# Optimization experiments

Hardware: AMD Instinct MI355X
Metric: run time of the kernel (lower is better)

The kernel has to match this reference:

```python
import jax, jax.numpy as jnp
import numpy as np

N_NODES = 100000
N_EDGES = 1600000
D = 128
K = 3
LEAKY_ALPHA = 0.2  # tf.nn.leaky_relu default
L2_EPS = 1e-12     # tf.math.l2_normalize default


def spmm(row, col, val, x, n_nodes):
    # y[r] = sum_{e: row[e]==r} val[e] * x[col[e]]
    return jax.ops.segment_sum(val[:, None] * x[col], row, num_segments=n_nodes)


def setup_inputs() -> dict:
    key = jax.random.key(0)
    ks = jax.random.split(key, 8)
    embeddings = jax.random.normal(ks[0], (N_NODES, D), dtype=jnp.float32) * 0.1
    edge_row = jax.random.randint(ks[1], (N_EDGES,), 0, N_NODES, dtype=jnp.int32)
    edge_col = jax.random.randint(ks[2], (N_EDGES,), 0, N_NODES, dtype=jnp.int32)
    # normalized-laplacian-like positive weights
    edge_val = jax.random.uniform(ks[3], (N_EDGES,), dtype=jnp.float32) * 0.05
    W_gc = jax.random.normal(ks[4], (K, D, D), dtype=jnp.float32) * (1.0 / np.sqrt(D))
    b_gc = jax.random.normal(ks[5], (K, D), dtype=jnp.float32) * 0.01
    W_bi = jax.random.normal(ks[6], (K, D, D), dtype=jnp.float32) * (1.0 / np.sqrt(D))
    b_bi = jax.random.normal(ks[7], (K, D), dtype=jnp.float32) * 0.01
    return {"embeddings": embeddings, "edge_row": edge_row, "edge_col": edge_col,
            "edge_val": edge_val, "W_gc": W_gc, "b_gc": b_gc, "W_bi": W_bi, "b_bi": b_bi}


def reference(embeddings, edge_row, edge_col, edge_val, W_gc, b_gc, W_bi, b_bi):
    n = embeddings.shape[0]
    x = embeddings
    depth_embeddings = [x]
    for i in range(W_gc.shape[0]):
        Lx = spmm(edge_row, edge_col, edge_val, x, n)   # L @ x  (L has zero diag)
        prop = Lx + x                                    # S @ x, S = L with diag 1
        emb = prop @ W_gc[i] + b_gc[i][None, :]
        bi = (x * Lx) @ W_bi[i] + b_bi[i][None, :]
        x = jax.nn.leaky_relu(emb + bi, negative_slope=LEAKY_ALPHA)
        sq = jnp.sum(x * x, axis=1, keepdims=True)
        norm_x = x / jnp.sqrt(jnp.maximum(sq, L2_EPS))   # tf l2_normalize semantics
        depth_embeddings.append(norm_x)
        x = norm_x  # note: original feeds normalized x to next layer via loop var? see notes
    return jnp.concatenate(depth_embeddings, axis=1)  # [N, (K+1)*D]
```

## Files before the change

### kernel.cpp

```cpp
#include <hip/hip_runtime.h>
#include <hip/hip_bf16.h>

#define ND 128
#define LDO 512
#define ALPHA 0.2f
#define L2EPS 1e-12f
#define SCAN_B 256
#define NCHUNK 256
#define RPB 512

typedef __attribute__((ext_vector_type(8))) short short8;
typedef __attribute__((ext_vector_type(4))) float f32x4;
typedef __attribute__((ext_vector_type(2))) float f32x2;

__device__ __forceinline__ short f2bf(float f) {
    union { float f; unsigned u; } c; c.f = f;
    unsigned u = c.u;
    unsigned r = (u + 0x7fffu + ((u >> 16) & 1u)) >> 16;
    return (short)r;
}
__device__ __forceinline__ float bf2f(unsigned short u) {
    union { unsigned u; float f; } c; c.u = ((unsigned)u) << 16;
    return c.f;
}
__device__ __forceinline__ void gload_lds16(const void* g, void* l) {
    __builtin_amdgcn_global_load_lds(
        (const __attribute__((address_space(1))) unsigned int*)g,
        (__attribute__((address_space(3))) unsigned int*)l, 16, 0, 0);
}

__global__ void copy_emb_kernel(const float* __restrict__ emb, float* __restrict__ out,
                                unsigned short* __restrict__ xb,
                                unsigned int* __restrict__ xf8w, int n) {
    int idx = blockIdx.x * blockDim.x + threadIdx.x;
    int total = n * 32;
    if (idx >= total) return;
    int r = idx >> 5, c4 = idx & 31;
    const float4 v = *reinterpret_cast<const float4*>(emb + (size_t)r * ND + c4 * 4);
    *reinterpret_cast<float4*>(out + (size_t)r * LDO + c4 * 4) = v;
    ushort4 b;
    b.x = (unsigned short)f2bf(v.x); b.y = (unsigned short)f2bf(v.y);
    b.z = (unsigned short)f2bf(v.z); b.w = (unsigned short)f2bf(v.w);
    *reinterpret_cast<ushort4*>(xb + (size_t)r * ND + c4 * 4) = b;
    unsigned int u = __builtin_amdgcn_cvt_pk_fp8_f32(v.x, v.y, 0, false);
    u = __builtin_amdgcn_cvt_pk_fp8_f32(v.z, v.w, u, true);
    xf8w[(size_t)r * 32 + c4] = u;
}

__global__ __launch_bounds__(256) void bucket_hist_kernel(const int* __restrict__ erow,
                                                          int* __restrict__ gcnt,
                                                          int n_edges, int nb, int ch) {
    __shared__ int cnt[256];
    int b = blockIdx.x;
    cnt[threadIdx.x] = 0;
    __syncthreads();
    int s = b * ch, e = min(n_edges, s + ch);
    for (int j = s + threadIdx.x; j < e; j += 256) {
        atomicAdd(&cnt[erow[j] >> 9], 1);
    }
    __syncthreads();
    for (int i = threadIdx.x; i < nb; i += 256) gcnt[i * NCHUNK + b] = cnt[i];
}

__global__ __launch_bounds__(SCAN_B) void scanA_kernel(const int* __restrict__ in,
                                                       int* __restrict__ outp,
                                                       int* __restrict__ partials, int n) {
    __shared__ int sm[SCAN_B];
    int i = blockIdx.x * SCAN_B + threadIdx.x;
    int v = (i < n) ? in[i] : 0;
    sm[threadIdx.x] = v;
    __syncthreads();
#pragma unroll
    for (int off = 1; off < SCAN_B; off <<= 1) {
        int t = (threadIdx.x >= off) ? sm[threadIdx.x - off] : 0;
        __syncthreads();
        sm[threadIdx.x] += t;
        __syncthreads();
    }
    if (i < n) outp[i] = sm[threadIdx.x] - v;
    if (threadIdx.x == SCAN_B - 1) partials[blockIdx.x] = sm[SCAN_B - 1];
}

__global__ __launch_bounds__(512) void scanB_kernel(int* __restrict__ partials, int nb) {
    __shared__ int sm[512];
    int v = (threadIdx.x < nb) ? partials[threadIdx.x] : 0;
    sm[threadIdx.x] = v;
    __syncthreads();
#pragma unroll
    for (int off = 1; off < 512; off <<= 1) {
        int t = (threadIdx.x >= off) ? sm[threadIdx.x - off] : 0;
        __syncthreads();
        sm[threadIdx.x] += t;
        __syncthreads();
    }
    if (threadIdx.x < nb) partials[threadIdx.x] = sm[threadIdx.x] - v;
}

__global__ __launch_bounds__(256) void bucket_scatter_kernel(const int* __restrict__ erow,
                                                             const int* __restrict__ ecol,
                                                             const float* __restrict__ eval,
                                                             const int* __restrict__ gscan,
                                                             const int* __restrict__ part,
                                                             int2* __restrict__ tmp,
                                                             int n_edges, int nb, int ch) {
    __shared__ int cur[256];
    int b = blockIdx.x;
    for (int i = threadIdx.x; i < nb; i += 256)
        cur[i] = gscan[i * NCHUNK + b] + part[i];
    __syncthreads();
    int s = b * ch, e = min(n_edges, s + ch);
    for (int j = s + threadIdx.x; j < e; j += 256) {
        int r = erow[j];
        int pos = atomicAdd(&cur[r >> 9], 1);
        int2 p;
        p.x = ecol[j] | ((r & (RPB - 1)) << 17);
        p.y = __float_as_int(eval[j]);
        tmp[pos] = p;
    }
}

__global__ __launch_bounds__(256) void bucket_sort_kernel(const int2* __restrict__ tmp,
                                                          const int* __restrict__ gscan,
                                                          const int* __restrict__ part,
                                                          int2* __restrict__ pv,
                                                          int* __restrict__ row_start,
                                                          int n, int n_edges, int nb) {
    __shared__ int hist[RPB];
    __shared__ int cur[RPB];
    __shared__ int sc[256];
    const int t = threadIdx.x;
    const int bkt = blockIdx.x;
    const int r0 = bkt << 9;
    const int s = gscan[bkt * NCHUNK] + part[bkt];
    const int e = (bkt + 1 < nb) ? (gscan[(bkt + 1) * NCHUNK] + part[bkt + 1]) : n_edges;

    for (int i = t; i < RPB; i += 256) hist[i] = 0;
    __syncthreads();
    for (int j = s + t; j < e; j += 256) atomicAdd(&hist[tmp[j].x >> 17], 1);
    __syncthreads();
    int a0 = hist[2 * t], a1 = hist[2 * t + 1];
    sc[t] = a0 + a1;
    __syncthreads();
#pragma unroll
    for (int off = 1; off < 256; off <<= 1) {
        int v = (t >= off) ? sc[t - off] : 0;
        __syncthreads();
        sc[t] += v;
        __syncthreads();
    }
    int base = s + sc[t] - a0 - a1;
    cur[2 * t] = base;
    cur[2 * t + 1] = base + a0;
    __syncthreads();
    int r1 = min(n, r0 + RPB);
    for (int i = t; i < r1 - r0; i += 256) row_start[r0 + i] = cur[i];
    if (t == 0 && r1 == n) row_start[n] = n_edges;
    __syncthreads();
    for (int j = s + t; j < e; j += 256) {
        int2 p = tmp[j];
        int pos = atomicAdd(&cur[p.x >> 17], 1);
        int2 q;
        q.x = p.x & 0x1FFFF;
        q.y = p.y;
        pv[pos] = q;
    }
}

__global__ __launch_bounds__(256) void spmm_axm_kernel(const int* __restrict__ row_start,
                                                       const int2* __restrict__ pv,
                                                       const unsigned char* __restrict__ xf8,
                                                       const unsigned short* __restrict__ xb,
                                                       unsigned short* __restrict__ Axm, int n) {
    int r = blockIdx.x * 16 + (threadIdx.x >> 4);
    if (r >= n) return;
    int l = threadIdx.x & 15;
    int s = row_start[r], e = row_start[r + 1];
    float a[8] = {0.f, 0.f, 0.f, 0.f, 0.f, 0.f, 0.f, 0.f};
    int j = s;
    for (; j + 3 < e; j += 4) {
        int2 p0 = pv[j], p1 = pv[j + 1], p2 = pv[j + 2], p3 = pv[j + 3];
        uint2 q0 = *reinterpret_cast<const uint2*>(xf8 + (size_t)p0.x * ND + l * 8);
        uint2 q1 = *reinterpret_cast<const uint2*>(xf8 + (size_t)p1.x * ND + l * 8);
        uint2 q2 = *reinterpret_cast<const uint2*>(xf8 + (size_t)p2.x * ND + l * 8);
        uint2 q3 = *reinterpret_cast<const uint2*>(xf8 + (size_t)p3.x * ND + l * 8);
        float v0 = __int_as_float(p0.y), v1 = __int_as_float(p1.y);
        float v2 = __int_as_float(p2.y), v3 = __int_as_float(p3.y);
        f32x2 g0 = __builtin_amdgcn_cvt_pk_f32_fp8(q0.x, false);
        f32x2 g1 = __builtin_amdgcn_cvt_pk_f32_fp8(q0.x, true);
        f32x2 g2 = __builtin_amdgcn_cvt_pk_f32_fp8(q0.y, false);
        f32x2 g3 = __builtin_amdgcn_cvt_pk_f32_fp8(q0.y, true);
        a[0] += v0 * g0.x; a[1] += v0 * g0.y; a[2] += v0 * g1.x; a[3] += v0 * g1.y;
        a[4] += v0 * g2.x; a[5] += v0 * g2.y; a[6] += v0 * g3.x; a[7] += v0 * g3.y;
        g0 = __builtin_amdgcn_cvt_pk_f32_fp8(q1.x, false);
        g1 = __builtin_amdgcn_cvt_pk_f32_fp8(q1.x, true);
        g2 = __builtin_amdgcn_cvt_pk_f32_fp8(q1.y, false);
        g3 = __builtin_amdgcn_cvt_pk_f32_fp8(q1.y, true);
        a[0] += v1 * g0.x; a[1] += v1 * g0.y; a[2] += v1 * g1.x; a[3] += v1 * g1.y;
        a[4] += v1 * g2.x; a[5] += v1 * g2.y; a[6] += v1 * g3.x; a[7] += v1 * g3.y;
        g0 = __builtin_amdgcn_cvt_pk_f32_fp8(q2.x, false);
        g1 = __builtin_amdgcn_cvt_pk_f32_fp8(q2.x, true);
        g2 = __builtin_amdgcn_cvt_pk_f32_fp8(q2.y, false);
        g3 = __builtin_amdgcn_cvt_pk_f32_fp8(q2.y, true);
        a[0] += v2 * g0.x; a[1] += v2 * g0.y; a[2] += v2 * g1.x; a[3] += v2 * g1.y;
        a[4] += v2 * g2.x; a[5] += v2 * g2.y; a[6] += v2 * g3.x; a[7] += v2 * g3.y;
        g0 = __builtin_amdgcn_cvt_pk_f32_fp8(q3.x, false);
        g1 = __builtin_amdgcn_cvt_pk_f32_fp8(q3.x, true);
        g2 = __builtin_amdgcn_cvt_pk_f32_fp8(q3.y, false);
        g3 = __builtin_amdgcn_cvt_pk_f32_fp8(q3.y, true);
        a[0] += v3 * g0.x; a[1] += v3 * g0.y; a[2] += v3 * g1.x; a[3] += v3 * g1.y;
        a[4] += v3 * g2.x; a[5] += v3 * g2.y; a[6] += v3 * g3.x; a[7] += v3 * g3.y;
    }
    for (; j < e; ++j) {
        int2 p0 = pv[j];
        float v0 = __int_as_float(p0.y);
        uint2 q0 = *reinterpret_cast<const uint2*>(xf8 + (size_t)p0.x * ND + l * 8);
        f32x2 g0 = __builtin_amdgcn_cvt_pk_f32_fp8(q0.x, false);
        f32x2 g1 = __builtin_amdgcn_cvt_pk_f32_fp8(q0.x, true);
        f32x2 g2 = __builtin_amdgcn_cvt_pk_f32_fp8(q0.y, false);
        f32x2 g3 = __builtin_amdgcn_cvt_pk_f32_fp8(q0.y, true);
        a[0] += v0 * g0.x; a[1] += v0 * g0.y;
        a[2] += v0 * g1.x; a[3] += v0 * g1.y;
        a[4] += v0 * g2.x; a[5] += v0 * g2.y;
        a[6] += v0 * g3.x; a[7] += v0 * g3.y;
    }
    short8 xv = *reinterpret_cast<const short8*>(xb + (size_t)r * ND + l * 8);
    short8 prv, xmv;
#pragma unroll
    for (int q = 0; q < 8; ++q) {
        float xf = bf2f((unsigned short)xv[q]);
        prv[q] = f2bf(xf + a[q]);
        xmv[q] = f2bf(xf * a[q]);
    }
    int sz = r & 7;
    unsigned short* rowp = Axm + (size_t)r * 256;
    *reinterpret_cast<short8*>(rowp + ((l        ^ sz) << 3)) = prv;
    *reinterpret_cast<short8*>(rowp + (((16 + l) ^ sz) << 3)) = xmv;
}

__global__ void prep_w_kernel(const float* __restrict__ Wgc, const float* __restrict__ bgc,
                              const float* __restrict__ Wbi, const float* __restrict__ bbi,
                              short* __restrict__ Wt2, float* __restrict__ bsum) {
    int z = blockIdx.x;
    int k = blockIdx.y;
    int t = threadIdx.x;
    int nn = t & 127;
    int h  = (t < 128) ? 0 : 1;
    const float* src = h ? (Wbi + ((size_t)z * 128 + k) * 128)
                         : (Wgc + ((size_t)z * 128 + k) * 128);
    float v = src[nn];
    int idx16 = k >> 3, e8 = k & 7;
    size_t addr = ((size_t)(z * 2 + h) * 128 + nn) * 128 + ((idx16 ^ (nn & 7)) << 3) + e8;
    Wt2[addr] = f2bf(v);
    if (k == 0 && t < 128) bsum[z * 128 + t] = bgc[z * 128 + t] + bbi[z * 128 + t];
}

__global__ __launch_bounds__(256) void fused_layer_mfma(
        const unsigned short* __restrict__ Axm,
        const short* __restrict__ Wt2,
        const float* __restrict__ bsum,
        float* __restrict__ xout,
        unsigned short* __restrict__ xbout,
        unsigned char* __restrict__ xf8out,
        int n) {
    __shared__ short A_lds[64 * 256];
    __shared__ short W_lds[128 * 128];

    const int tid  = threadIdx.x;
    const int row0 = blockIdx.x * 64;
    const int lane = tid & 63;
    const int w    = tid >> 6;
    const int lrow = lane & 15;
    const int kgrp = lane >> 4;

    {
        const char* gA = (const char*)(Axm + (size_t)row0 * 256) + w * 8192 + lane * 16;
        char*       lA = (char*)A_lds + w * 8192;
        const char* gW = (const char*)Wt2 + w * 8192 + lane * 16;
        char*       lW = (char*)W_lds + w * 8192;
#pragma unroll
        for (int it = 0; it < 8; ++it) {
            gload_lds16(gA + it * 1024, lA + it * 1024);
            gload_lds16(gW + it * 1024, lW + it * 1024);
        }
    }
    asm volatile("s_waitcnt vmcnt(0)" ::: "memory");
    __syncthreads();

    f32x4 acc[8];
#pragma unroll
    for (int nf = 0; nf < 8; ++nf) acc[nf] = (f32x4){0.f, 0.f, 0.f, 0.f};

    const int ar  = w * 16 + lrow;
    const int as_ = ar & 7;

#pragma unroll
    for (int ksl = 0; ksl < 4; ++ksl) {
        int kkl = ksl * 4 + kgrp;
        short8 af = *reinterpret_cast<const short8*>(&A_lds[ar * 256 + ((kkl ^ as_) << 3)]);
#pragma unroll
        for (int nf = 0; nf < 8; ++nf) {
            int nr = nf * 16 + lrow;
            short8 bfr = *reinterpret_cast<const short8*>(&W_lds[nr * 128 + ((kkl ^ (nr & 7)) << 3)]);
            acc[nf] = __builtin_amdgcn_mfma_f32_16x16x32_bf16(af, bfr, acc[nf], 0, 0, 0);
        }
    }
    __syncthreads();
    {
        const char* gW = (const char*)Wt2 + 32768 + w * 8192 + lane * 16;
        char*       lW = (char*)W_lds + w * 8192;
#pragma unroll
        for (int it = 0; it < 8; ++it) gload_lds16(gW + it * 1024, lW + it * 1024);
    }
    asm volatile("s_waitcnt vmcnt(0)" ::: "memory");
    __syncthreads();

#pragma unroll
    for (int ksl = 0; ksl < 4; ++ksl) {
        int kkl = ksl * 4 + kgrp;
        short8 af = *reinterpret_cast<const short8*>(&A_lds[ar * 256 + (((16 + kkl) ^ as_) << 3)]);
#pragma unroll
        for (int nf = 0; nf < 8; ++nf) {
            int nr = nf * 16 + lrow;
            short8 bfr = *reinterpret_cast<const short8*>(&W_lds[nr * 128 + ((kkl ^ (nr & 7)) << 3)]);
            acc[nf] = __builtin_amdgcn_mfma_f32_16x16x32_bf16(af, bfr, acc[nf], 0, 0, 0);
        }
    }

    float bsv[8];
#pragma unroll
    for (int nf = 0; nf < 8; ++nf) bsv[nf] = bsum[nf * 16 + lrow];

#pragma unroll
    for (int reg = 0; reg < 4; ++reg) {
        int grow = row0 + w * 16 + kgrp * 4 + reg;
        float v[8];
        float ssq = 0.f;
#pragma unroll
        for (int nf = 0; nf < 8; ++nf) {
            float tv = acc[nf][reg] + bsv[nf];
            tv = tv > 0.f ? tv : ALPHA * tv;
            v[nf] = tv;
            ssq += tv * tv;
        }
        ssq += __shfl_xor(ssq, 1);
        ssq += __shfl_xor(ssq, 2);
        ssq += __shfl_xor(ssq, 4);
        ssq += __shfl_xor(ssq, 8);
        float sc = 1.0f / sqrtf(fmaxf(ssq, L2EPS));
        if (grow < n) {
            float* op = xout + (size_t)grow * LDO;
            unsigned short* bp = xbout + (size_t)grow * ND;
            unsigned char* fp = xf8out + (size_t)grow * ND;
#pragma unroll
            for (int nf = 0; nf < 8; ++nf) {
                float ov = v[nf] * sc;
                __builtin_nontemporal_store(ov, op + nf * 16 + lrow);
                bp[nf * 16 + lrow] = (unsigned short)f2bf(ov);
                unsigned int u8 = __builtin_amdgcn_cvt_pk_fp8_f32(ov, ov, 0, false);
                fp[nf * 16 + lrow] = (unsigned char)(u8 & 0xff);
            }
        }
    }
}

extern "C" void kernel_launch(void* const* d_in, const int* in_sizes, int n_in,
                              void* d_out, int out_size, void* d_ws, size_t ws_size,
                              hipStream_t stream) {
    const float* emb  = (const float*)d_in[0];
    const int*   erow = (const int*)d_in[1];
    const int*   ecol = (const int*)d_in[2];
    const float* eval = (const float*)d_in[3];
    const float* Wgc  = (const float*)d_in[4];
    const float* bgc  = (const float*)d_in[5];
    const float* Wbi  = (const float*)d_in[6];
    const float* bbi  = (const float*)d_in[7];
    float* out = (float*)d_out;

    const int n        = in_sizes[0] / ND;
    const int n_edges  = in_sizes[1];
    const int n_layers = in_sizes[5] / ND;

    const int nb = (n + RPB - 1) >> 9;
    const int ch = (n_edges + NCHUNK - 1) / NCHUNK;
    const int ng = nb * NCHUNK;

    char* ws = (char*)d_ws;
    size_t off = 0;
    auto alloc = [&](size_t bytes) { void* p = ws + off; off = (off + bytes + 255) & ~(size_t)255; return p; };
    unsigned short* xb  = (unsigned short*)alloc((size_t)n * ND * sizeof(short));
    unsigned char*  xf8 = (unsigned char*) alloc((size_t)n * ND);
    unsigned short* Axm = (unsigned short*)alloc((size_t)(n + 64) * 256 * sizeof(short));
    int2*  pv        = (int2*) alloc((size_t)n_edges * sizeof(int2));
    int2*  tmp       = (int2*) alloc((size_t)n_edges * sizeof(int2));
    int*   row_start = (int*)  alloc((size_t)(n + 1) * sizeof(int));
    int*   gcnt      = (int*)  alloc((size_t)ng * sizeof(int));
    int*   gscan     = (int*)  alloc((size_t)ng * sizeof(int));
    int*   partials  = (int*)  alloc(512 * sizeof(int));
    short* Wt2       = (short*)alloc((size_t)n_layers * 2 * 128 * 128 * sizeof(short));
    float* bsum      = (float*)alloc((size_t)n_layers * 128 * sizeof(float));
    (void)ws_size;

    {
        int total = n * 32;
        copy_emb_kernel<<<(total + 255) / 256, 256, 0, stream>>>(emb, out, xb,
                                                                 (unsigned int*)xf8, n);
    }

    {
        dim3 g(n_layers, 128);
        prep_w_kernel<<<g, 256, 0, stream>>>(Wgc, bgc, Wbi, bbi, Wt2, bsum);
    }

    bucket_hist_kernel<<<NCHUNK, 256, 0, stream>>>(erow, gcnt, n_edges, nb, ch);
    {
        int nblk = (ng + SCAN_B - 1) / SCAN_B;
        scanA_kernel<<<nblk, SCAN_B, 0, stream>>>(gcnt, gscan, partials, ng);
        scanB_kernel<<<1, 512, 0, stream>>>(partials, nblk);
    }
    bucket_scatter_kernel<<<NCHUNK, 256, 0, stream>>>(erow, ecol, eval, gscan, partials,
                                                      tmp, n_edges, nb, ch);
    bucket_sort_kernel<<<nb, 256, 0, stream>>>(tmp, gscan, partials, pv, row_start,
                                               n, n_edges, nb);

    for (int i = 0; i < n_layers; ++i) {
        spmm_axm_kernel<<<(n + 15) / 16, 256, 0, stream>>>(row_start, pv, xf8, xb, Axm, n);
        fused_layer_mfma<<<(n + 63) / 64, 256, 0, stream>>>(
            Axm, Wt2 + (size_t)i * 2 * 128 * 128, bsum + (size_t)i * 128,
            out + (size_t)(i + 1) * ND, xb, xf8, n);
    }
}
```

Before: 328.6 us.

## Sort rows by degree and use 8 lanes per row in SpMM

Builds a degree histogram during the bucket sort, then scans and scatters it into a row permutation so each SpMM wavefront handles rows of similar degree, which reduces load imbalance within a warp. The SpMM kernel now maps 8 lanes per row, each loading 16 fp8 bytes per neighbour, so each block covers 32 rows instead of 16. This adds three small preprocessing launches and a memset. It also loses the locality of contiguous row order for the output and x reads, since rows are now visited in permuted order.

```diff
diff --git a/kernel.cpp b/kernel.cpp
--- a/kernel.cpp
+++ b/kernel.cpp
@@ -8,6 +8,7 @@
 #define SCAN_B 256
 #define NCHUNK 256
 #define RPB 512
+#define DBIN 1024
 
 typedef __attribute__((ext_vector_type(8))) short short8;
 typedef __attribute__((ext_vector_type(4))) float f32x4;
@@ -124,6 +125,7 @@
                                                           const int* __restrict__ part,
                                                           int2* __restrict__ pv,
                                                           int* __restrict__ row_start,
+                                                          int* __restrict__ deg_hist,
                                                           int n, int n_edges, int nb) {
     __shared__ int hist[RPB];
     __shared__ int cur[RPB];
@@ -139,6 +141,8 @@
     for (int j = s + t; j < e; j += 256) atomicAdd(&hist[tmp[j].x >> 17], 1);
     __syncthreads();
     int a0 = hist[2 * t], a1 = hist[2 * t + 1];
+    if (r0 + 2 * t < n)     atomicAdd(&deg_hist[min(a0, DBIN - 1)], 1);
+    if (r0 + 2 * t + 1 < n) atomicAdd(&deg_hist[min(a1, DBIN - 1)], 1);
     sc[t] = a0 + a1;
     __syncthreads();
 #pragma unroll
@@ -166,75 +170,118 @@
     }
 }
 
+__global__ __launch_bounds__(DBIN) void deg_scan_kernel(int* __restrict__ deg) {
+    __shared__ int sm[DBIN];
+    int t = threadIdx.x;
+    int v = deg[t];
+    sm[t] = v;
+    __syncthreads();
+#pragma unroll
+    for (int off = 1; off < DBIN; off <<= 1) {
+        int u = (t >= off) ? sm[t - off] : 0;
+        __syncthreads();
+        sm[t] += u;
+        __syncthreads();
+    }
+    deg[t] = sm[t] - v;
+}
+
+__global__ __launch_bounds__(256) void deg_scatter_kernel(const int* __restrict__ row_start,
+                                                          int* __restrict__ deg_base,
+                                                          int* __restrict__ rowperm, int n) {
+    __shared__ int lh[DBIN];
+    __shared__ int lbase[DBIN];
+    int t = threadIdx.x;
+    for (int i = t; i < DBIN; i += 256) lh[i] = 0;
+    __syncthreads();
+    int r = blockIdx.x * 256 + t;
+    int d = 0, lpos = 0;
+    bool valid = (r < n);
+    if (valid) {
+        d = min(row_start[r + 1] - row_start[r], DBIN - 1);
+        lpos = atomicAdd(&lh[d], 1);
+    }
+    __syncthreads();
+    for (int i = t; i < DBIN; i += 256) {
+        int c = lh[i];
+        if (c) lbase[i] = atomicAdd(&deg_base[i], c);
+    }
+    __syncthreads();
+    if (valid) rowperm[lbase[d] + lpos] = r;
+}
+
 __global__ __launch_bounds__(256) void spmm_axm_kernel(const int* __restrict__ row_start,
+                                                       const int* __restrict__ rowperm,
                                                        const int2* __restrict__ pv,
                                                        const unsigned char* __restrict__ xf8,
                                                        const unsigned short* __restrict__ xb,
                                                        unsigned short* __restrict__ Axm, int n) {
-    int r = blockIdx.x * 16 + (threadIdx.x >> 4);
-    if (r >= n) return;
-    int l = threadIdx.x & 15;
+    int idx = blockIdx.x * 32 + (threadIdx.x >> 3);
+    if (idx >= n) return;
+    int r = rowperm[idx];
+    int l = threadIdx.x & 7;
     int s = row_start[r], e = row_start[r + 1];
-    float a[8] = {0.f, 0.f, 0.f, 0.f, 0.f, 0.f, 0.f, 0.f};
+    float a[16];
+#pragma unroll
+    for (int q = 0; q < 16; ++q) a[q] = 0.f;
     int j = s;
-    for (; j + 3 < e; j += 4) {
-        int2 p0 = pv[j], p1 = pv[j + 1], p2 = pv[j + 2], p3 = pv[j + 3];
-        uint2 q0 = *reinterpret_cast<const uint2*>(xf8 + (size_t)p0.x * ND + l * 8);
-        uint2 q1 = *reinterpret_cast<const uint2*>(xf8 + (size_t)p1.x * ND + l * 8);
-        uint2 q2 = *reinterpret_cast<const uint2*>(xf8 + (size_t)p2.x * ND + l * 8);
-        uint2 q3 = *reinterpret_cast<const uint2*>(xf8 + (size_t)p3.x * ND + l * 8);
+    for (; j + 1 < e; j += 2) {
+        int2 p0 = pv[j], p1 = pv[j + 1];
+        uint4 q0 = *reinterpret_cast<const uint4*>(xf8 + (size_t)p0.x * ND + l * 16);
+        uint4 q1 = *reinterpret_cast<const uint4*>(xf8 + (size_t)p1.x * ND + l * 16);
         float v0 = __int_as_float(p0.y), v1 = __int_as_float(p1.y);
-        float v2 = __int_as_float(p2.y), v3 = __int_as_float(p3.y);
-        f32x2 g0 = __builtin_amdgcn_cvt_pk_f32_fp8(q0.x, false);
-        f32x2 g1 = __builtin_amdgcn_cvt_pk_f32_fp8(q0.x, true);
-        f32x2 g2 = __builtin_amdgcn_cvt_pk_f32_fp8(q0.y, false);
-        f32x2 g3 = __builtin_amdgcn_cvt_pk_f32_fp8(q0.y, true);
-        a[0] += v0 * g0.x; a[1] += v0 * g0.y; a[2] += v0 * g1.x; a[3] += v0 * g1.y;
-        a[4] += v0 * g2.x; a[5] += v0 * g2.y; a[6] += v0 * g3.x; a[7] += v0 * g3.y;
-        g0 = __builtin_amdgcn_cvt_pk_f32_fp8(q1.x, false);
-        g1 = __builtin_amdgcn_cvt_pk_f32_fp8(q1.x, true);
-        g2 = __builtin_amdgcn_cvt_pk_f32_fp8(q1.y, false);
-        g3 = __builtin_amdgcn_cvt_pk_f32_fp8(q1.y, true);
-        a[0] += v1 * g0.x; a[1] += v1 * g0.y; a[2] += v1 * g1.x; a[3] += v1 * g1.y;
-        a[4] += v1 * g2.x; a[5] += v1 * g2.y; a[6] += v1 * g3.x; a[7] += v1 * g3.y;
-        g0 = __builtin_amdgcn_cvt_pk_f32_fp8(q2.x, false);
-        g1 = __builtin_amdgcn_cvt_pk_f32_fp8(q2.x, true);
-        g2 = __builtin_amdgcn_cvt_pk_f32_fp8(q2.y, false);
-        g3 = __builtin_amdgcn_cvt_pk_f32_fp8(q2.y, true);
-        a[0] += v2 * g0.x; a[1] += v2 * g0.y; a[2] += v2 * g1.x; a[3] += v2 * g1.y;
-        a[4] += v2 * g2.x; a[5] += v2 * g2.y; a[6] += v2 * g3.x; a[7] += v2 * g3.y;
-        g0 = __builtin_amdgcn_cvt_pk_f32_fp8(q3.x, false);
-        g1 = __builtin_amdgcn_cvt_pk_f32_fp8(q3.x, true);
-        g2 = __builtin_amdgcn_cvt_pk_f32_fp8(q3.y, false);
-        g3 = __builtin_amdgcn_cvt_pk_f32_fp8(q3.y, true);
-        a[0] += v3 * g0.x; a[1] += v3 * g0.y; a[2] += v3 * g1.x; a[3] += v3 * g1.y;
-        a[4] += v3 * g2.x; a[5] += v3 * g2.y; a[6] += v3 * g3.x; a[7] += v3 * g3.y;
-    }
-    for (; j < e; ++j) {
+        f32x2 c;
+        c = __builtin_amdgcn_cvt_pk_f32_fp8(q0.x, false); a[0]  += v0 * c.x; a[1]  += v0 * c.y;
+        c = __builtin_amdgcn_cvt_pk_f32_fp8(q0.x, true);  a[2]  += v0 * c.x; a[3]  += v0 * c.y;
+        c = __builtin_amdgcn_cvt_pk_f32_fp8(q0.y, false); a[4]  += v0 * c.x; a[5]  += v0 * c.y;
+        c = __builtin_amdgcn_cvt_pk_f32_fp8(q0.y, true);  a[6]  += v0 * c.x; a[7]  += v0 * c.y;
+        c = __builtin_amdgcn_cvt_pk_f32_fp8(q0.z, false); a[8]  += v0 * c.x; a[9]  += v0 * c.y;
+        c = __builtin_amdgcn_cvt_pk_f32_fp8(q0.z, true);  a[10] += v0 * c.x; a[11] += v0 * c.y;
+        c = __builtin_amdgcn_cvt_pk_f32_fp8(q0.w, false); a[12] += v0 * c.x; a[13] += v0 * c.y;
+        c = __builtin_amdgcn_cvt_pk_f32_fp8(q0.w, true);  a[14] += v0 * c.x; a[15] += v0 * c.y;
+        c = __builtin_amdgcn_cvt_pk_f32_fp8(q1.x, false); a[0]  += v1 * c.x; a[1]  += v1 * c.y;
+        c = __builtin_amdgcn_cvt_pk_f32_fp8(q1.x, true);  a[2]  += v1 * c.x; a[3]  += v1 * c.y;
+        c = __builtin_amdgcn_cvt_pk_f32_fp8(q1.y, false); a[4]  += v1 * c.x; a[5]  += v1 * c.y;
+        c = __builtin_amdgcn_cvt_pk_f32_fp8(q1.y, true);  a[6]  += v1 * c.x; a[7]  += v1 * c.y;
+        c = __builtin_amdgcn_cvt_pk_f32_fp8(q1.z, false); a[8]  += v1 * c.x; a[9]  += v1 * c.y;
+        c = __builtin_amdgcn_cvt_pk_f32_fp8(q1.z, true);  a[10] += v1 * c.x; a[11] += v1 * c.y;
+        c = __builtin_amdgcn_cvt_pk_f32_fp8(q1.w, false); a[12] += v1 * c.x; a[13] += v1 * c.y;
+        c = __builtin_amdgcn_cvt_pk_f32_fp8(q1.w, true);  a[14] += v1 * c.x; a[15] += v1 * c.y;
+    }
+    if (j < e) {
         int2 p0 = pv[j];
+        uint4 q0 = *reinterpret_cast<const uint4*>(xf8 + (size_t)p0.x * ND + l * 16);
         float v0 = __int_as_float(p0.y);
-        uint2 q0 = *reinterpret_cast<const uint2*>(xf8 + (size_t)p0.x * ND + l * 8);
-        f32x2 g0 = __builtin_amdgcn_cvt_pk_f32_fp8(q0.x, false);
-        f32x2 g1 = __builtin_amdgcn_cvt_pk_f32_fp8(q0.x, true);
-        f32x2 g2 = __builtin_amdgcn_cvt_pk_f32_fp8(q0.y, false);
-        f32x2 g3 = __builtin_amdgcn_cvt_pk_f32_fp8(q0.y, true);
-        a[0] += v0 * g0.x; a[1] += v0 * g0.y;
-        a[2] += v0 * g1.x; a[3] += v0 * g1.y;
-        a[4] += v0 * g2.x; a[5] += v0 * g2.y;
-        a[6] += v0 * g3.x; a[7] += v0 * g3.y;
-    }
-    short8 xv = *reinterpret_cast<const short8*>(xb + (size_t)r * ND + l * 8);
-    short8 prv, xmv;
+        f32x2 c;
+        c = __builtin_amdgcn_cvt_pk_f32_fp8(q0.x, false); a[0]  += v0 * c.x; a[1]  += v0 * c.y;
+        c = __builtin_amdgcn_cvt_pk_f32_fp8(q0.x, true);  a[2]  += v0 * c.x; a[3]  += v0 * c.y;
+        c = __builtin_amdgcn_cvt_pk_f32_fp8(q0.y, false); a[4]  += v0 * c.x; a[5]  += v0 * c.y;
+        c = __builtin_amdgcn_cvt_pk_f32_fp8(q0.y, true);  a[6]  += v0 * c.x; a[7]  += v0 * c.y;
+        c = __builtin_amdgcn_cvt_pk_f32_fp8(q0.z, false); a[8]  += v0 * c.x; a[9]  += v0 * c.y;
+        c = __builtin_amdgcn_cvt_pk_f32_fp8(q0.z, true);  a[10] += v0 * c.x; a[11] += v0 * c.y;
+        c = __builtin_amdgcn_cvt_pk_f32_fp8(q0.w, false); a[12] += v0 * c.x; a[13] += v0 * c.y;
+        c = __builtin_amdgcn_cvt_pk_f32_fp8(q0.w, true);  a[14] += v0 * c.x; a[15] += v0 * c.y;
+    }
+    const unsigned short* xr = xb + (size_t)r * ND + l * 16;
+    short8 xv0 = *reinterpret_cast<const short8*>(xr);
+    short8 xv1 = *reinterpret_cast<const short8*>(xr + 8);
+    short8 pr0, pr1, xm0, xm1;
 #pragma unroll
     for (int q = 0; q < 8; ++q) {
-        float xf = bf2f((unsigned short)xv[q]);
-        prv[q] = f2bf(xf + a[q]);
-        xmv[q] = f2bf(xf * a[q]);
+        float x0 = bf2f((unsigned short)xv0[q]);
+        float x1 = bf2f((unsigned short)xv1[q]);
+        pr0[q] = f2bf(x0 + a[q]);
+        xm0[q] = f2bf(x0 * a[q]);
+        pr1[q] = f2bf(x1 + a[8 + q]);
+        xm1[q] = f2bf(x1 * a[8 + q]);
     }
     int sz = r & 7;
+    int c0 = 2 * l, c1 = 2 * l + 1;
     unsigned short* rowp = Axm + (size_t)r * 256;
-    *reinterpret_cast<short8*>(rowp + ((l        ^ sz) << 3)) = prv;
-    *reinterpret_cast<short8*>(rowp + (((16 + l) ^ sz) << 3)) = xmv;
+    *reinterpret_cast<short8*>(rowp + ((c0        ^ sz) << 3)) = pr0;
+    *reinterpret_cast<short8*>(rowp + ((c1        ^ sz) << 3)) = pr1;
+    *reinterpret_cast<short8*>(rowp + (((16 + c0) ^ sz) << 3)) = xm0;
+    *reinterpret_cast<short8*>(rowp + (((16 + c1) ^ sz) << 3)) = xm1;
 }
 
 __global__ void prep_w_kernel(const float* __restrict__ Wgc, const float* __restrict__ bgc,
@@ -393,9 +440,11 @@
     int2*  pv        = (int2*) alloc((size_t)n_edges * sizeof(int2));
     int2*  tmp       = (int2*) alloc((size_t)n_edges * sizeof(int2));
     int*   row_start = (int*)  alloc((size_t)(n + 1) * sizeof(int));
+    int*   rowperm   = (int*)  alloc((size_t)n * sizeof(int));
     int*   gcnt      = (int*)  alloc((size_t)ng * sizeof(int));
     int*   gscan     = (int*)  alloc((size_t)ng * sizeof(int));
     int*   partials  = (int*)  alloc(512 * sizeof(int));
+    int*   deg_hist  = (int*)  alloc(DBIN * sizeof(int));
     short* Wt2       = (short*)alloc((size_t)n_layers * 2 * 128 * 128 * sizeof(short));
     float* bsum      = (float*)alloc((size_t)n_layers * 128 * sizeof(float));
     (void)ws_size;
@@ -411,6 +460,7 @@
         prep_w_kernel<<<g, 256, 0, stream>>>(Wgc, bgc, Wbi, bbi, Wt2, bsum);
     }
 
+    hipMemsetAsync(deg_hist, 0, DBIN * sizeof(int), stream);
     bucket_hist_kernel<<<NCHUNK, 256, 0, stream>>>(erow, gcnt, n_edges, nb, ch);
     {
         int nblk = (ng + SCAN_B - 1) / SCAN_B;
@@ -420,10 +470,13 @@
     bucket_scatter_kernel<<<NCHUNK, 256, 0, stream>>>(erow, ecol, eval, gscan, partials,
                                                       tmp, n_edges, nb, ch);
     bucket_sort_kernel<<<nb, 256, 0, stream>>>(tmp, gscan, partials, pv, row_start,
-                                               n, n_edges, nb);
+                                               deg_hist, n, n_edges, nb);
+    deg_scan_kernel<<<1, DBIN, 0, stream>>>(deg_hist);
+    deg_scatter_kernel<<<(n + 255) / 256, 256, 0, stream>>>(row_start, deg_hist, rowperm, n);
 
     for (int i = 0; i < n_layers; ++i) {
-        spmm_axm_kernel<<<(n + 15) / 16, 256, 0, stream>>>(row_start, pv, xf8, xb, Axm, n);
+        spmm_axm_kernel<<<(n + 31) / 32, 256, 0, stream>>>(row_start, rowperm, pv, xf8, xb,
+                                                           Axm, n);
         fused_layer_mfma<<<(n + 63) / 64, 256, 0, stream>>>(
             Axm, Wt2 + (size_t)i * 2 * 128 * 128, bsum + (size_t)i * 128,
             out + (size_t)(i + 1) * ND, xb, xf8, n);
```

After: 587.9 us. +78.9%, slower.
